# Performance work log

Hardware: AMD Instinct MI355X
Metric: run time of the kernel (lower is better)

Reference implementation:

```python
import jax, jax.numpy as jnp
import numpy as np

D_MODEL = 512
N_HEADS = 8
MAX_DEPTH = 4
D_FF = 4 * D_MODEL
B, L = 4, 2048


def setup_inputs() -> dict:
    key = jax.random.key(0)
    ks = jax.random.split(key, 16)
    s = 0.02
    inp = {
        "x": jax.random.normal(ks[0], (B, L, D_MODEL), dtype=jnp.float32),
        # attention pre-norm
        "ln1_g": jnp.ones((D_MODEL,), jnp.float32),
        "ln1_b": jnp.zeros((D_MODEL,), jnp.float32),
        # MultiheadAttention in_proj (3D, D) and out_proj (D, D), torch (out, in) layout
        "Wqkv": jax.random.normal(ks[1], (3 * D_MODEL, D_MODEL), jnp.float32) * s,
        "bqkv": jnp.zeros((3 * D_MODEL,), jnp.float32),
        "Wo": jax.random.normal(ks[2], (D_MODEL, D_MODEL), jnp.float32) * s,
        "bo": jnp.zeros((D_MODEL,), jnp.float32),
        # FFN pre-norm + MLP
        "ln2_g": jnp.ones((D_MODEL,), jnp.float32),
        "ln2_b": jnp.zeros((D_MODEL,), jnp.float32),
        "W1": jax.random.normal(ks[3], (D_FF, D_MODEL), jnp.float32) * s,
        "b1": jnp.zeros((D_FF,), jnp.float32),
        "W2": jax.random.normal(ks[4], (D_MODEL, D_FF), jnp.float32) * s,
        "b2": jnp.zeros((D_MODEL,), jnp.float32),
        # token-choice depth router: LayerNorm + Linear(D,D) + GELU + Linear(D,max_depth)
        "rn_g": jnp.ones((D_MODEL,), jnp.float32),
        "rn_b": jnp.zeros((D_MODEL,), jnp.float32),
        "Rw1": jax.random.normal(ks[5], (D_MODEL, D_MODEL), jnp.float32) * s,
        "Rb1": jnp.zeros((D_MODEL,), jnp.float32),
        "Rw2": jax.random.normal(ks[6], (MAX_DEPTH, D_MODEL), jnp.float32) * s,
        "Rb2": jnp.zeros((MAX_DEPTH,), jnp.float32),
    }
    return inp


def _layernorm(x, g, b, eps=1e-5):
    mu = jnp.mean(x, axis=-1, keepdims=True)
    var = jnp.var(x, axis=-1, keepdims=True)
    return (x - mu) * jax.lax.rsqrt(var + eps) * g + b


def _block(x, ln1_g, ln1_b, Wqkv, bqkv, Wo, bo, ln2_g, ln2_b, W1, b1, W2, b2):
    Bb, Ll, D = x.shape
    H = N_HEADS
    dh = D // H
    # pre-norm self-attention
    h = _layernorm(x, ln1_g, ln1_b)
    qkv = h @ Wqkv.T + bqkv                      # (B, L, 3D)
    q, k, v = jnp.split(qkv, 3, axis=-1)
    q = q.reshape(Bb, Ll, H, dh)
    k = k.reshape(Bb, Ll, H, dh)
    v = v.reshape(Bb, Ll, H, dh)
    scores = jnp.einsum("blhd,bmhd->bhlm", q, k) / jnp.sqrt(jnp.float32(dh))
    attn = jax.nn.softmax(scores, axis=-1)
    o = jnp.einsum("bhlm,bmhd->blhd", attn, v).reshape(Bb, Ll, D)
    x = x + (o @ Wo.T + bo)
    # pre-norm FFN (exact-erf GELU, matching torch nn.GELU default)
    h2 = _layernorm(x, ln2_g, ln2_b)
    f = jax.nn.gelu(h2 @ W1.T + b1, approximate=False) @ W2.T + b2
    return x + f


def reference(x, ln1_g, ln1_b, Wqkv, bqkv, Wo, bo, ln2_g, ln2_b, W1, b1, W2, b2,
              rn_g, rn_b, Rw1, Rb1, Rw2, Rb2):
    # --- token-choice depth router (eval mode: argmax) ---
    rh = _layernorm(x, rn_g, rn_b)
    rh = jax.nn.gelu(rh @ Rw1.T + Rb1, approximate=False)
    router_logits = rh @ Rw2.T + Rb2             # (B, L, MAX_DEPTH)
    depths = jnp.argmax(router_logits, axis=-1) + 1  # (B, L) in [1, MAX_DEPTH]
    # --- dense recursion with torch.where-style selection ---
    cur = x
    for level in range(1, MAX_DEPTH + 1):
        upd = _block(cur, ln1_g, ln1_b, Wqkv, bqkv, Wo, bo,
                     ln2_g, ln2_b, W1, b1, W2, b2)
        keep = (depths >= level)[..., None]      # (B, L, 1)
        cur = jnp.where(keep, upd, cur)
    return cur, depths, router_logits
```

## Files before the change

### kernel.cpp

```cpp
#include <hip/hip_runtime.h>

typedef unsigned short u16;
typedef __attribute__((ext_vector_type(8))) short short8;
typedef __attribute__((ext_vector_type(4))) short s16x4;
typedef __attribute__((ext_vector_type(4))) float floatx4;
typedef __attribute__((ext_vector_type(4))) unsigned short u16x4;

#define NTOK 8192
#define DMODEL 512
#define DFF 2048
#define LSEQ 2048
#define RMARGIN 1e-3f

__device__ __forceinline__ u16 f2bf(float f) {
    union { float f; unsigned u; } x; x.f = f;
    unsigned r = (x.u + 0x7fffu + ((x.u >> 16) & 1u)) >> 16;
    return (u16)r;
}
__device__ __forceinline__ float bf2f(u16 h) {
    union { unsigned u; float f; } x; x.u = ((unsigned)h) << 16;
    return x.f;
}

__device__ __forceinline__ float geluf(float x) {
    return 0.5f * x * (1.0f + erff(x * 0.70710678118654752f));
}

__device__ __forceinline__ void gload_lds16(const void* g, void* l) {
    __builtin_amdgcn_global_load_lds(
        (const __attribute__((address_space(1))) void*)g,
        (__attribute__((address_space(3))) void*)l,
        16, 0, 0);
}

__device__ __forceinline__ s16x4 pack_p(float p0, float p1, float p2, float p3) {
    union { float f; unsigned u; } a{p0}, b{p1}, c{p2}, d{p3};
    union { unsigned u[2]; s16x4 s; } r;
    r.u[0] = (a.u >> 16) | (b.u & 0xffff0000u);
    r.u[1] = (c.u >> 16) | (d.u & 0xffff0000u);
    return r.s;
}

__global__ __launch_bounds__(256) void cvt_w(const float* __restrict__ wq,
                                             const float* __restrict__ wo,
                                             const float* __restrict__ w1,
                                             const float* __restrict__ w2,
                                             u16* __restrict__ out) {
    int i = blockIdx.x * 256 + threadIdx.x;
    float v;
    if (i < 786432)       v = wq[i];
    else if (i < 1048576) v = wo[i - 786432];
    else if (i < 2097152) v = w1[i - 1048576];
    else                  v = w2[i - 2097152];
    out[i] = f2bf(v);
}

__global__ __launch_bounds__(256) void copy_f32(const float* __restrict__ a,
                                                float* __restrict__ b) {
    size_t i = ((size_t)blockIdx.x * 256 + threadIdx.x) * 4;
    *(floatx4*)&b[i] = *(const floatx4*)&a[i];
}

__global__ __launch_bounds__(256) void cvt_rw1(const float* __restrict__ Rw1,
                                               u16* __restrict__ out) {
    const int i = blockIdx.x * 256 + threadIdx.x;
    const int n = i >> 9, k = i & 511;
    const float v = Rw1[i];
    const u16 hi = f2bf(v);
    const u16 lo = f2bf(v - bf2f(hi));
    out[(size_t)n * 1536 + k] = hi;
    out[(size_t)n * 1536 + 512 + k] = hi;
    out[(size_t)n * 1536 + 1024 + k] = lo;
}

__global__ __launch_bounds__(256) void cvt_split(const float* __restrict__ x,
                                                 u16* __restrict__ out,
                                                 int* __restrict__ cnt) {
    if (blockIdx.x == 0 && threadIdx.x == 0) *cnt = 0;
    const int i = blockIdx.x * 256 + threadIdx.x;
    const int base = i * 4;
    const int row = base >> 9, k = base & 511;
    const floatx4 v = *(const floatx4*)&x[base];
    u16x4 h, l;
#pragma unroll
    for (int e = 0; e < 4; ++e) {
        h[e] = f2bf(v[e]);
        l[e] = f2bf(v[e] - bf2f(h[e]));
    }
    u16* o = out + (size_t)row * 1536;
    *(u16x4*)&o[k] = h;
    *(u16x4*)&o[512 + k] = l;
    *(u16x4*)&o[1024 + k] = h;
}

template<bool OUTF32>
__global__ __launch_bounds__(256)
void ln_k(const float* __restrict__ x, const float* __restrict__ g,
          const float* __restrict__ bb, void* __restrict__ outp) {
    const int row = blockIdx.x * 4 + (threadIdx.x >> 6);
    const int lane = threadIdx.x & 63;
    const float* xr = x + (size_t)row * DMODEL;
    const int c0 = lane * 4, c1 = c0 + 256;
    floatx4 a = *(const floatx4*)&xr[c0];
    floatx4 b = *(const floatx4*)&xr[c1];
    float s = 0.f, sq = 0.f;
#pragma unroll
    for (int e = 0; e < 4; ++e) { s += a[e]; sq += a[e] * a[e]; }
#pragma unroll
    for (int e = 0; e < 4; ++e) { s += b[e]; sq += b[e] * b[e]; }
#pragma unroll
    for (int m = 32; m >= 1; m >>= 1) {
        s += __shfl_xor(s, m);
        sq += __shfl_xor(sq, m);
    }
    const float mean = s * (1.f / 512.f);
    const float rstd = rsqrtf(sq * (1.f / 512.f) - mean * mean + 1e-5f);
    floatx4 g0 = *(const floatx4*)&g[c0];
    floatx4 g1 = *(const floatx4*)&g[c1];
    floatx4 b0 = *(const floatx4*)&bb[c0];
    floatx4 b1 = *(const floatx4*)&bb[c1];
    floatx4 y0, y1;
#pragma unroll
    for (int e = 0; e < 4; ++e) {
        y0[e] = (a[e] - mean) * rstd * g0[e] + b0[e];
        y1[e] = (b[e] - mean) * rstd * g1[e] + b1[e];
    }
    if (OUTF32) {
        float* o = (float*)outp + (size_t)row * DMODEL;
        *(floatx4*)&o[c0] = y0;
        *(floatx4*)&o[c1] = y1;
    } else {
        u16* o = (u16*)outp + (size_t)row * DMODEL;
        u16x4 p0, p1;
#pragma unroll
        for (int e = 0; e < 4; ++e) { p0[e] = f2bf(y0[e]); p1[e] = f2bf(y1[e]); }
        *(u16x4*)&o[c0] = p0;
        *(u16x4*)&o[c1] = p1;
    }
}

template<int EPI, int BN>
__global__ __launch_bounds__(256, 2)
void gemm_bt(const u16* __restrict__ A, const u16* __restrict__ Bw,
             const float* __restrict__ bias,
             u16* __restrict__ Cb, float* __restrict__ Cf,
             const float* __restrict__ res, const float* __restrict__ depth,
             u16* __restrict__ Cv,
             float aux, int N, int K) {
    constexpr int NJ = BN / 32;
    __shared__ __align__(16) u16 As[128 * 32];
    __shared__ __align__(16) u16 Bs[BN * 32];
    const int tid = threadIdx.x;
    const int lane = tid & 63;
    const int w = tid >> 6;
    const int wm = (w >> 1) * 64;
    const int wn = (w & 1) * (BN / 2);
    const int mBase = blockIdx.x * 128;
    const int nBase = blockIdx.y * BN;
    const int q4 = lane >> 4, rl = lane & 15;

    floatx4 acc[4][NJ];
#pragma unroll
    for (int i = 0; i < 4; ++i)
#pragma unroll
        for (int j = 0; j < NJ; ++j) acc[i][j] = (floatx4){0.f, 0.f, 0.f, 0.f};

    const int i0 = tid, i1 = tid + 256;
    const int ar0 = i0 >> 2, ac0 = ((i0 & 3) ^ ((i0 >> 3) & 3)) * 8;
    const int ar1 = i1 >> 2, ac1 = ((i1 & 3) ^ ((i1 >> 3) & 3)) * 8;
    const u16* pA0 = A + (size_t)(mBase + ar0) * K + ac0;
    const u16* pA1 = A + (size_t)(mBase + ar1) * K + ac1;
    const u16* pB0 = Bw + (size_t)(nBase + ar0) * K + ac0;
    const u16* pB1 = (BN == 128) ? Bw + (size_t)(nBase + ar1) * K + ac1 : pB0;
    u16* lA0 = &As[i0 * 8];
    u16* lA1 = &As[i1 * 8];
    u16* lB0 = &Bs[i0 * 8];
    u16* lB1 = (BN == 128) ? &Bs[i1 * 8] : lB0;

    for (int k0 = 0; k0 < K; k0 += 32) {
        gload_lds16(pA0, lA0);
        gload_lds16(pA1, lA1);
        gload_lds16(pB0, lB0);
        if (BN == 128) gload_lds16(pB1, lB1);
        pA0 += 32; pA1 += 32; pB0 += 32;
        if (BN == 128) pB1 += 32;
        __syncthreads();
        short8 af[4], bf[NJ];
#pragma unroll
        for (int t = 0; t < 4; ++t) {
            const int r = wm + t * 16 + rl;
            af[t] = *(const short8*)&As[r * 32 + (q4 ^ ((r >> 1) & 3)) * 8];
        }
#pragma unroll
        for (int t = 0; t < NJ; ++t) {
            const int r = wn + t * 16 + rl;
            bf[t] = *(const short8*)&Bs[r * 32 + (q4 ^ ((r >> 1) & 3)) * 8];
        }
#pragma unroll
        for (int ti = 0; ti < 4; ++ti)
#pragma unroll
            for (int tj = 0; tj < NJ; ++tj)
                acc[ti][tj] = __builtin_amdgcn_mfma_f32_16x16x32_bf16(
                    af[ti], bf[tj], acc[ti][tj], 0, 0, 0);
        __syncthreads();
    }

#pragma unroll
    for (int ti = 0; ti < 4; ++ti) {
        const int r0 = mBase + wm + ti * 16 + q4 * 4;
#pragma unroll
        for (int tj = 0; tj < NJ; ++tj) {
            const int c = nBase + wn + tj * 16 + rl;
            const float bv = bias[c];
            if (EPI == 0) {
                if (nBase < 1024) {
                    const float sc = (nBase < 512) ? aux : 1.0f;
#pragma unroll
                    for (int rr = 0; rr < 4; ++rr)
                        Cb[(size_t)(r0 + rr) * 1024 + c] =
                            f2bf((acc[ti][tj][rr] + bv) * sc);
                } else {
                    const int cm = c - 1024;
                    const int hh = cm >> 6, dh = cm & 63;
                    const int bb2 = r0 >> 11, kv = r0 & 2047;
                    u16x4 pk;
#pragma unroll
                    for (int rr = 0; rr < 4; ++rr)
                        pk[rr] = f2bf(acc[ti][tj][rr] + bv);
                    *(u16x4*)&Cv[((size_t)(bb2 * 8 + hh) * 64 + dh) * 2048 + kv] = pk;
                }
            } else {
#pragma unroll
                for (int rr = 0; rr < 4; ++rr) {
                    const int r = r0 + rr;
                    const float v = acc[ti][tj][rr] + bv;
                    if (EPI == 1) {
                        Cb[(size_t)r * N + c] = f2bf(geluf(v));
                    } else if (EPI == 2) {
                        Cf[(size_t)r * N + c] = res[(size_t)r * N + c] + v;
                    } else if (EPI == 3) {
                        if (depth[r] >= aux)
                            Cf[(size_t)r * N + c] = res[(size_t)r * N + c] + v;
                    } else {
                        Cf[(size_t)r * N + c] = geluf(v);
                    }
                }
            }
        }
    }
}

__global__ __launch_bounds__(256, 4)
void attn_k(const u16* __restrict__ qk, const u16* __restrict__ vT,
            u16* __restrict__ o) {
    const int qt = blockIdx.x;
    const int bh = blockIdx.y;
    const int b = bh >> 3, h = bh & 7;
    const int tid = threadIdx.x, lane = tid & 63, w = tid >> 6;
    const int tok0 = b * LSEQ;
    const int qrow0 = qt * 64 + w * 16;
    const int q4 = lane >> 4, rl = lane & 15;

    __shared__ __align__(16) u16 Kt[128 * 64];
    __shared__ __align__(16) u16 Vt[64 * 128];

    const u16* vbase = vT + (size_t)bh * 64 * 2048;

    short8 qf[2];
#pragma unroll
    for (int ks = 0; ks < 2; ++ks)
        qf[ks] = *(const short8*)&qk[(size_t)(tok0 + qrow0 + rl) * 1024
                                      + h * 64 + ks * 32 + q4 * 8];

    floatx4 oacc[4];
#pragma unroll
    for (int dt = 0; dt < 4; ++dt) oacc[dt] = (floatx4){0.f, 0.f, 0.f, 0.f};
    float lsum = 0.f;

    for (int kt = 0; kt < 16; ++kt) {
        const int kv0 = kt * 128;
        __syncthreads();
#pragma unroll
        for (int it = 0; it < 4; ++it) {
            const int i = it * 256 + tid;
            const int r = i >> 3;
            const int c = ((i & 7) ^ (r & 7)) * 8;
            gload_lds16(&qk[(size_t)(tok0 + kv0 + r) * 1024 + 512 + h * 64 + c],
                        &Kt[i * 8]);
        }
#pragma unroll
        for (int it = 0; it < 4; ++it) {
            const int i = it * 256 + tid;
            const int dh = i >> 4;
            const int ch = (i & 15) ^ (dh & 15);
            gload_lds16(&vbase[(size_t)dh * 2048 + kv0 + ch * 8], &Vt[i * 8]);
        }
        __syncthreads();

#pragma unroll
        for (int mt = 0; mt < 8; ++mt) {
            const int r = mt * 16 + rl;
            short8 kf0 = *(const short8*)&Kt[r * 64 + ((q4) ^ (r & 7)) * 8];
            short8 kf1 = *(const short8*)&Kt[r * 64 + ((4 + q4) ^ (r & 7)) * 8];
            floatx4 s;
            s = __builtin_amdgcn_mfma_f32_16x16x32_bf16(kf0, qf[0],
                    (floatx4){0.f, 0.f, 0.f, 0.f}, 0, 0, 0);
            s = __builtin_amdgcn_mfma_f32_16x16x32_bf16(kf1, qf[1], s, 0, 0, 0);
            const float p0 = exp2f(s[0]);
            const float p1 = exp2f(s[1]);
            const float p2 = exp2f(s[2]);
            const float p3 = exp2f(s[3]);
            lsum += (p0 + p1) + (p2 + p3);
            const s16x4 pb = pack_p(p0, p1, p2, p3);
            const int ct = 2 * mt + (q4 >> 1);
#pragma unroll
            for (int dt = 0; dt < 4; ++dt) {
                const s16x4 vf = *(const s16x4*)&Vt[(dt * 16 + rl) * 128
                                                    + (ct ^ rl) * 8 + (q4 & 1) * 4];
                oacc[dt] = __builtin_amdgcn_mfma_f32_16x16x16bf16_1k(
                    vf, pb, oacc[dt], 0, 0, 0);
            }
        }
    }

    float l = lsum;
    l += __shfl_xor(l, 16);
    l += __shfl_xor(l, 32);
    const float inv = 1.0f / l;
    const size_t row = tok0 + qrow0 + rl;
#pragma unroll
    for (int dt = 0; dt < 4; ++dt) {
        u16x4 pk;
#pragma unroll
        for (int rr = 0; rr < 4; ++rr) pk[rr] = f2bf(oacc[dt][rr] * inv);
        *(u16x4*)&o[row * DMODEL + h * 64 + dt * 16 + q4 * 4] = pk;
    }
}

__global__ __launch_bounds__(256)
void router_logits_f32(const float* __restrict__ rr, const float* __restrict__ Rw2,
                       const float* __restrict__ Rb2, float* __restrict__ logits,
                       float* __restrict__ depthf, int* __restrict__ cnt,
                       int* __restrict__ list) {
    const int t = blockIdx.x * 4 + (threadIdx.x >> 6);
    const int lane = threadIdx.x & 63;
    const float* xr = rr + (size_t)t * 512;
    const int c0 = lane * 4, c1 = c0 + 256;
    floatx4 a = *(const floatx4*)&xr[c0];
    floatx4 b = *(const floatx4*)&xr[c1];
    float s[4];
#pragma unroll
    for (int d = 0; d < 4; ++d) {
        const float* wr = Rw2 + d * 512;
        floatx4 wa = *(const floatx4*)&wr[c0];
        floatx4 wb = *(const floatx4*)&wr[c1];
        float acc = 0.f;
#pragma unroll
        for (int e = 0; e < 4; ++e) acc += a[e] * wa[e];
#pragma unroll
        for (int e = 0; e < 4; ++e) acc += b[e] * wb[e];
        s[d] = acc;
    }
#pragma unroll
    for (int m = 32; m >= 1; m >>= 1)
#pragma unroll
        for (int d = 0; d < 4; ++d) s[d] += __shfl_xor(s[d], m);
    if (lane == 0) {
        float v[4];
        float bv = -1e30f; int best = 0;
#pragma unroll
        for (int d = 0; d < 4; ++d) {
            v[d] = s[d] + Rb2[d];
            logits[(size_t)t * 4 + d] = v[d];
            if (v[d] > bv) { bv = v[d]; best = d; }
        }
        float second = -1e30f;
#pragma unroll
        for (int d = 0; d < 4; ++d)
            if (d != best) second = fmaxf(second, v[d]);
        depthf[t] = (float)(best + 1);
        if (bv - second < RMARGIN) {
            int idx = atomicAdd(cnt, 1);
            list[idx] = t;
        }
    }
}

__global__ __launch_bounds__(256)
void router_exact(const float* __restrict__ rh, const float* __restrict__ Rw1,
                  const float* __restrict__ Rb1, const float* __restrict__ Rw2,
                  const float* __restrict__ Rb2, const int* __restrict__ cnt,
                  const int* __restrict__ list, float* __restrict__ logits,
                  float* __restrict__ depthf) {
    __shared__ float rhs[512];
    __shared__ double rrd[512];
    __shared__ double lg[4];
    const int n = *cnt;
    const int tid = threadIdx.x;
    for (int ii = blockIdx.x; ii < n; ii += gridDim.x) {
        const int t = list[ii];
        rhs[tid] = rh[(size_t)t * 512 + tid];
        rhs[tid + 256] = rh[(size_t)t * 512 + 256 + tid];
        __syncthreads();
#pragma unroll
        for (int oo = 0; oo < 2; ++oo) {
            const int nn = tid + oo * 256;
            double acc = (double)Rb1[nn];
            const float* wrow = Rw1 + (size_t)nn * 512;
            for (int k = 0; k < 512; ++k)
                acc = fma((double)rhs[k], (double)wrow[k], acc);
            rrd[nn] = 0.5 * acc * (1.0 + erf(acc * 0.70710678118654752440));
        }
        __syncthreads();
        const int w = tid >> 6, lane = tid & 63;
        double acc2 = 0.0;
        for (int k = lane; k < 512; k += 64)
            acc2 += rrd[k] * (double)Rw2[w * 512 + k];
#pragma unroll
        for (int m = 32; m >= 1; m >>= 1) acc2 += __shfl_xor(acc2, m);
        if (lane == 0) lg[w] = acc2 + (double)Rb2[w];
        __syncthreads();
        if (tid == 0) {
            double bv = -1e300; int best = 0;
#pragma unroll
            for (int d = 0; d < 4; ++d) {
                const double v = lg[d];
                logits[(size_t)t * 4 + d] = (float)v;
                if (v > bv) { bv = v; best = d; }
            }
            depthf[t] = (float)(best + 1);
        }
        __syncthreads();
    }
}

extern "C" void kernel_launch(void* const* d_in, const int* in_sizes, int n_in,
                              void* d_out, int out_size, void* d_ws, size_t ws_size,
                              hipStream_t stream) {
    (void)in_sizes; (void)n_in; (void)out_size; (void)ws_size;
    const float* x    = (const float*)d_in[0];
    const float* ln1g = (const float*)d_in[1];
    const float* ln1b = (const float*)d_in[2];
    const float* Wqkv = (const float*)d_in[3];
    const float* bqkv = (const float*)d_in[4];
    const float* Wo   = (const float*)d_in[5];
    const float* bo   = (const float*)d_in[6];
    const float* ln2g = (const float*)d_in[7];
    const float* ln2b = (const float*)d_in[8];
    const float* W1   = (const float*)d_in[9];
    const float* b1   = (const float*)d_in[10];
    const float* W2   = (const float*)d_in[11];
    const float* b2   = (const float*)d_in[12];
    const float* rng  = (const float*)d_in[13];
    const float* rnb  = (const float*)d_in[14];
    const float* Rw1  = (const float*)d_in[15];
    const float* Rb1  = (const float*)d_in[16];
    const float* Rw2  = (const float*)d_in[17];
    const float* Rb2  = (const float*)d_in[18];

    float* cur    = (float*)d_out;
    float* depthf = cur + (size_t)NTOK * DMODEL;
    float* logits = depthf + NTOK;

    char* ws = (char*)d_ws;
    float* xmid = (float*)ws;
    u16* sbuf   = (u16*)(ws + 16777216);
    u16* qk     = (u16*)(ws + 25165824);
    u16* ffb    = (u16*)(ws + 41943040);
    u16* vTb    = (u16*)(ws + 75497472);
    u16* wbf    = (u16*)(ws + 83886080);

    u16* rw1s   = (u16*)(ws + 16777216);
    int* rcnt   = (int*)(ws + 18874368);
    int* rlist  = rcnt + 16;
    u16* asplit = ffb;
    float* rrf  = (float*)qk;

    u16* wq = wbf;
    u16* wo = wbf + 786432;
    u16* w1 = wbf + 1048576;
    u16* w2 = wbf + 2097152;

    const float qsc = 0.125f * 1.4426950408889634f;

    cvt_w<<<12288, 256, 0, stream>>>(Wqkv, Wo, W1, W2, wbf);
    copy_f32<<<4096, 256, 0, stream>>>(x, cur);

    ln_k<true><<<2048, 256, 0, stream>>>(x, rng, rnb, xmid);
    cvt_rw1<<<1024, 256, 0, stream>>>(Rw1, rw1s);
    cvt_split<<<4096, 256, 0, stream>>>(xmid, asplit, rcnt);
    gemm_bt<4, 64><<<dim3(64, 8), 256, 0, stream>>>(
        asplit, rw1s, Rb1, nullptr, rrf, nullptr, nullptr, nullptr, 0.f, 512, 1536);
    router_logits_f32<<<2048, 256, 0, stream>>>(rrf, Rw2, Rb2, logits, depthf,
                                                rcnt, rlist);
    router_exact<<<128, 256, 0, stream>>>(xmid, Rw1, Rb1, Rw2, Rb2, rcnt, rlist,
                                          logits, depthf);

    for (int level = 1; level <= 4; ++level) {
        ln_k<false><<<2048, 256, 0, stream>>>(cur, ln1g, ln1b, sbuf);
        gemm_bt<0, 128><<<dim3(64, 12), 256, 0, stream>>>(
            sbuf, wq, bqkv, qk, nullptr, nullptr, nullptr, vTb, qsc, 1536, 512);
        attn_k<<<dim3(32, 32), 256, 0, stream>>>(qk, vTb, sbuf);
        gemm_bt<2, 64><<<dim3(64, 8), 256, 0, stream>>>(
            sbuf, wo, bo, nullptr, xmid, cur, nullptr, nullptr, 0.f, 512, 512);
        ln_k<false><<<2048, 256, 0, stream>>>(xmid, ln2g, ln2b, sbuf);
        gemm_bt<1, 128><<<dim3(64, 16), 256, 0, stream>>>(
            sbuf, w1, b1, ffb, nullptr, nullptr, nullptr, nullptr, 0.f, 2048, 512);
        gemm_bt<3, 64><<<dim3(64, 8), 256, 0, stream>>>(
            ffb, w2, b2, nullptr, cur, xmid, depthf, nullptr, (float)level, 512, 2048);
    }
}
```

Before: 907.6 us.

## Process two query tiles per wave in attention to reuse K/V fragments

Each wave in the attention kernel now handles 32 query rows (two 16-row tiles) instead of 16, so every K and V fragment read from LDS feeds two MFMAs. Each block now loads its K/V tile once for 128 queries, which halves the global-to-LDS K/V traffic and the LDS reads per query. The cost is more registers per thread (launch bounds lowered to 2 blocks per SM) and half as many blocks (512), which may hurt occupancy and latency hiding.

```diff
diff --git a/kernel.cpp b/kernel.cpp
--- a/kernel.cpp
+++ b/kernel.cpp
@@ -250,7 +250,7 @@
     }
 }
 
-__global__ __launch_bounds__(256, 4)
+__global__ __launch_bounds__(256, 2)
 void attn_k(const u16* __restrict__ qk, const u16* __restrict__ vT,
             u16* __restrict__ o) {
     const int qt = blockIdx.x;
@@ -258,7 +258,7 @@
     const int b = bh >> 3, h = bh & 7;
     const int tid = threadIdx.x, lane = tid & 63, w = tid >> 6;
     const int tok0 = b * LSEQ;
-    const int qrow0 = qt * 64 + w * 16;
+    const int qrow0 = qt * 128 + w * 32;
     const int q4 = lane >> 4, rl = lane & 15;
 
     __shared__ __align__(16) u16 Kt[128 * 64];
@@ -266,16 +266,23 @@
 
     const u16* vbase = vT + (size_t)bh * 64 * 2048;
 
-    short8 qf[2];
-#pragma unroll
-    for (int ks = 0; ks < 2; ++ks)
-        qf[ks] = *(const short8*)&qk[(size_t)(tok0 + qrow0 + rl) * 1024
-                                      + h * 64 + ks * 32 + q4 * 8];
-
-    floatx4 oacc[4];
-#pragma unroll
-    for (int dt = 0; dt < 4; ++dt) oacc[dt] = (floatx4){0.f, 0.f, 0.f, 0.f};
-    float lsum = 0.f;
+    short8 qf[2][2];
+#pragma unroll
+    for (int nt = 0; nt < 2; ++nt)
+#pragma unroll
+        for (int ks = 0; ks < 2; ++ks)
+            qf[nt][ks] = *(const short8*)&qk[(size_t)(tok0 + qrow0 + nt * 16 + rl) * 1024
+                                             + h * 64 + ks * 32 + q4 * 8];
+
+    floatx4 oacc[4][2];
+#pragma unroll
+    for (int dt = 0; dt < 4; ++dt)
+#pragma unroll
+        for (int nt = 0; nt < 2; ++nt) oacc[dt][nt] = (floatx4){0.f, 0.f, 0.f, 0.f};
+    float lsum[2] = {0.f, 0.f};
+
+    const u16* kp0 = &Kt[rl * 64 + ((q4 ^ (rl & 7))) * 8];
+    const u16* kp1 = &Kt[rl * 64 + (((4 + q4) ^ (rl & 7))) * 8];
 
     for (int kt = 0; kt < 16; ++kt) {
         const int kv0 = kt * 128;
@@ -299,41 +306,53 @@
 
 #pragma unroll
         for (int mt = 0; mt < 8; ++mt) {
-            const int r = mt * 16 + rl;
-            short8 kf0 = *(const short8*)&Kt[r * 64 + ((q4) ^ (r & 7)) * 8];
-            short8 kf1 = *(const short8*)&Kt[r * 64 + ((4 + q4) ^ (r & 7)) * 8];
-            floatx4 s;
-            s = __builtin_amdgcn_mfma_f32_16x16x32_bf16(kf0, qf[0],
-                    (floatx4){0.f, 0.f, 0.f, 0.f}, 0, 0, 0);
-            s = __builtin_amdgcn_mfma_f32_16x16x32_bf16(kf1, qf[1], s, 0, 0, 0);
-            const float p0 = exp2f(s[0]);
-            const float p1 = exp2f(s[1]);
-            const float p2 = exp2f(s[2]);
-            const float p3 = exp2f(s[3]);
-            lsum += (p0 + p1) + (p2 + p3);
-            const s16x4 pb = pack_p(p0, p1, p2, p3);
+            const short8 kf0 = *(const short8*)&kp0[mt * 1024];
+            const short8 kf1 = *(const short8*)&kp1[mt * 1024];
+            floatx4 s[2];
+#pragma unroll
+            for (int nt = 0; nt < 2; ++nt) {
+                s[nt] = __builtin_amdgcn_mfma_f32_16x16x32_bf16(kf0, qf[nt][0],
+                        (floatx4){0.f, 0.f, 0.f, 0.f}, 0, 0, 0);
+                s[nt] = __builtin_amdgcn_mfma_f32_16x16x32_bf16(kf1, qf[nt][1],
+                        s[nt], 0, 0, 0);
+            }
+            s16x4 pb[2];
+#pragma unroll
+            for (int nt = 0; nt < 2; ++nt) {
+                const float p0 = exp2f(s[nt][0]);
+                const float p1 = exp2f(s[nt][1]);
+                const float p2 = exp2f(s[nt][2]);
+                const float p3 = exp2f(s[nt][3]);
+                lsum[nt] += (p0 + p1) + (p2 + p3);
+                pb[nt] = pack_p(p0, p1, p2, p3);
+            }
             const int ct = 2 * mt + (q4 >> 1);
+            const u16* vp = &Vt[(ct ^ rl) * 8 + (q4 & 1) * 4 + rl * 128];
 #pragma unroll
             for (int dt = 0; dt < 4; ++dt) {
-                const s16x4 vf = *(const s16x4*)&Vt[(dt * 16 + rl) * 128
-                                                    + (ct ^ rl) * 8 + (q4 & 1) * 4];
-                oacc[dt] = __builtin_amdgcn_mfma_f32_16x16x16bf16_1k(
-                    vf, pb, oacc[dt], 0, 0, 0);
+                const s16x4 vf = *(const s16x4*)&vp[dt * 2048];
+#pragma unroll
+                for (int nt = 0; nt < 2; ++nt)
+                    oacc[dt][nt] = __builtin_amdgcn_mfma_f32_16x16x16bf16_1k(
+                        vf, pb[nt], oacc[dt][nt], 0, 0, 0);
             }
         }
     }
 
-    float l = lsum;
-    l += __shfl_xor(l, 16);
-    l += __shfl_xor(l, 32);
-    const float inv = 1.0f / l;
-    const size_t row = tok0 + qrow0 + rl;
-#pragma unroll
-    for (int dt = 0; dt < 4; ++dt) {
-        u16x4 pk;
-#pragma unroll
-        for (int rr = 0; rr < 4; ++rr) pk[rr] = f2bf(oacc[dt][rr] * inv);
-        *(u16x4*)&o[row * DMODEL + h * 64 + dt * 16 + q4 * 4] = pk;
+#pragma unroll
+    for (int nt = 0; nt < 2; ++nt) {
+        float l = lsum[nt];
+        l += __shfl_xor(l, 16);
+        l += __shfl_xor(l, 32);
+        const float inv = 1.0f / l;
+        const size_t row = tok0 + qrow0 + nt * 16 + rl;
+#pragma unroll
+        for (int dt = 0; dt < 4; ++dt) {
+            u16x4 pk;
+#pragma unroll
+            for (int rr = 0; rr < 4; ++rr) pk[rr] = f2bf(oacc[dt][nt][rr] * inv);
+            *(u16x4*)&o[row * DMODEL + h * 64 + dt * 16 + q4 * 4] = pk;
+        }
     }
 }
 
@@ -500,7 +519,7 @@
         ln_k<false><<<2048, 256, 0, stream>>>(cur, ln1g, ln1b, sbuf);
         gemm_bt<0, 128><<<dim3(64, 12), 256, 0, stream>>>(
             sbuf, wq, bqkv, qk, nullptr, nullptr, nullptr, vTb, qsc, 1536, 512);
-        attn_k<<<dim3(32, 32), 256, 0, stream>>>(qk, vTb, sbuf);
+        attn_k<<<dim3(16, 32), 256, 0, stream>>>(qk, vTb, sbuf);
         gemm_bt<2, 64><<<dim3(64, 8), 256, 0, stream>>>(
             sbuf, wo, bo, nullptr, xmid, cur, nullptr, nullptr, 0.f, 512, 512);
         ln_k<false><<<2048, 256, 0, stream>>>(xmid, ln2g, ln2b, sbuf);
```

Measured after the change: 913.8 us. No clear change (+0.7%).
